# Kernel optimization log

Measured on AMD Instinct MI355X. Metric: run time of the kernel, lower is better.

## Reference

```python
import jax, jax.numpy as jnp
import numpy as np

B, T, I, H, F = 32, 1024, 64, 512, 63
NEG = -1e9


def _init_params(key):
    ks = jax.random.split(key, 16)
    s = 0.02
    p = {}
    # LSTM (pytorch gate order i,f,g,o)
    p['w_ih'] = jax.random.normal(ks[0], (4 * H, I), jnp.float32) * s
    p['w_hh'] = jax.random.normal(ks[1], (4 * H, H), jnp.float32) * s
    p['b_ih'] = jnp.zeros((4 * H,), jnp.float32)
    p['b_hh'] = jnp.zeros((4 * H,), jnp.float32)
    # shared layer
    p['w_sh'] = jax.random.normal(ks[2], (H, H), jnp.float32) * s
    p['b_sh'] = jnp.zeros((H,), jnp.float32)
    # state attention: Linear(H,H) -> tanh -> Linear(H,1)
    p['w_sa'] = jax.random.normal(ks[3], (H, H), jnp.float32) * s
    p['b_sa'] = jnp.zeros((H,), jnp.float32)
    p['v_sa'] = jax.random.normal(ks[4], (1, H), jnp.float32) * s
    p['bv_sa'] = jnp.zeros((1,), jnp.float32)
    # reward attention
    p['w_ra'] = jax.random.normal(ks[5], (H, H), jnp.float32) * s
    p['b_ra'] = jnp.zeros((H,), jnp.float32)
    p['v_ra'] = jax.random.normal(ks[6], (1, H), jnp.float32) * s
    p['bv_ra'] = jnp.zeros((1,), jnp.float32)
    # heads
    p['w_st'] = jax.random.normal(ks[7], (F, H), jnp.float32) * s
    p['b_st'] = jnp.zeros((F,), jnp.float32)
    p['w_rw'] = jax.random.normal(ks[8], (1, H), jnp.float32) * s
    p['b_rw'] = jnp.zeros((1,), jnp.float32)
    return p


def setup_inputs() -> dict:
    key = jax.random.key(0)
    k1, k2, k3, kp = jax.random.split(key, 4)
    inp = {
        'x': jax.random.normal(k1, (B, T, I), jnp.float32),
        'x_lengths': jnp.full((B,), T, dtype=jnp.int64),  # full lengths: pack/pad is identity
        'h0': jax.random.normal(k2, (B, H), jnp.float32),
        'c0': jax.random.normal(k3, (B, H), jnp.float32),
    }
    inp.update(_init_params(kp))
    return inp


def _lstm(x, h0, c0, w_ih, w_hh, b_ih, b_hh):
    # x: [B,T,I] -> outputs [B,T,H], final (h,c)
    def step(carry, xt):
        h, c = carry
        gates = xt @ w_ih.T + h @ w_hh.T + b_ih + b_hh  # [B,4H]
        i, f, g, o = jnp.split(gates, 4, axis=-1)
        c = jax.nn.sigmoid(f) * c + jax.nn.sigmoid(i) * jnp.tanh(g)
        h = jax.nn.sigmoid(o) * jnp.tanh(c)
        return (h, c), h
    (hT, cT), outs = jax.lax.scan(step, (h0, c0), jnp.swapaxes(x, 0, 1))
    return jnp.swapaxes(outs, 0, 1), hT, cT


def _causal_attn(feat, w1, b1, v, bv):
    # additive attention pooling over every causal prefix, vectorized over t.
    e = jnp.tanh(feat @ w1.T + b1) @ v.T + bv        # [B,T,1]
    e = e[..., 0]                                     # [B,T]
    t = feat.shape[1]
    causal = jnp.tril(jnp.ones((t, t), bool))         # [T,T] j<=t
    logits = jnp.where(causal[None], e[:, None, :], NEG)
    w = jax.nn.softmax(logits, axis=-1)               # [B,T,T]
    return jnp.einsum('btj,bjh->bth', w, feat)        # [B,T,H]


def reference(x, x_lengths, h0, c0, w_ih, w_hh, b_ih, b_hh, w_sh, b_sh,
              w_sa, b_sa, v_sa, bv_sa, w_ra, b_ra, v_ra, bv_ra,
              w_st, b_st, w_rw, b_rw):
    r_out, hT, cT = _lstm(x, h0, c0, w_ih, w_hh, b_ih, b_hh)
    shared = r_out @ w_sh.T + b_sh                    # [B,T,H]
    state_ctx = _causal_attn(shared, w_sa, b_sa, v_sa, bv_sa)
    reward_ctx = _causal_attn(shared, w_ra, b_ra, v_ra, bv_ra)
    state_outs = state_ctx @ w_st.T + b_st            # [B,T,F]
    reward_outs = reward_ctx @ w_rw.T + b_rw          # [B,T,1]
    return state_outs, reward_outs, (hT, cT)
```

## Files before the change

### kernel.cpp

```cpp
#include <hip/hip_runtime.h>

#define BB 32
#define TT 1024
#define II 64
#define HH 512
#define FF 63
#define G4H 2048
#define KK 576
#define MM 32768
#define NW 32

#define RW_OFF 2064384
#define HT_OFF 2097152
#define CT_OFF 2113536

#define WS_FLAGS   0
#define WS_FLAG    4096
#define WS_TICK    4224
#define WS_CHOSEN  4288
#define WS_TICK2   4352
#define WS_BIASC   8448
#define WS_BSH     16640
#define WS_BCSA    18688
#define WS_BCRA    20736
#define WS_BCH     22784
#define WS_SCAL    23040
#define WS_VS      23168
#define WS_VR      24192
#define WS_ZB      25216
#define WS_H0      27264
#define WS_CP      60032
#define WS_WHPAD   92800
#define WS_WHC     223872
#define WS_WSHT    354944
#define WS_WSA     879232
#define WS_WRA     1403520
#define WS_WCSA    1927808
#define WS_WCRA    2452096
#define WS_WCAT    2976384
#define WS_XP      5335680
#define WS_ES      9529984
#define WS_ER      9661056
#define WS_PROJ    9792128
#define WS_HX      13986432

typedef __bf16  bf16x8 __attribute__((ext_vector_type(8)));
typedef float   f32x4  __attribute__((ext_vector_type(4)));
typedef uint4 uint4a __attribute__((may_alias));
typedef unsigned int u32;

__device__ __forceinline__ float bf2f(unsigned short u) {
    unsigned int v = ((unsigned int)u) << 16;
    return __builtin_bit_cast(float, v);
}
__device__ __forceinline__ unsigned short f2bf(float f) {
    unsigned int u = __builtin_bit_cast(unsigned int, f);
    u += 0x7fffu + ((u >> 16) & 1u);
    return (unsigned short)(u >> 16);
}
__device__ __forceinline__ bf16x8 ldb8(const unsigned short* p) {
    uint4 v = *(const uint4a*)p;
    return __builtin_bit_cast(bf16x8, v);
}
__device__ __forceinline__ float sigf(float x) { return 1.f / (1.f + __expf(-x)); }
__device__ __forceinline__ float tanhfast(float x) { return 1.f - 2.f / (__expf(2.f * x) + 1.f); }

__device__ __forceinline__ unsigned short loadu(const void* p, int i, int fl) {
    return fl ? f2bf(((const float*)p)[i]) : ((const unsigned short*)p)[i];
}
__device__ __forceinline__ float loadf(const void* p, int i, int fl) {
    return fl ? ((const float*)p)[i] : bf2f(((const unsigned short*)p)[i]);
}

__global__ void sniff_k(const unsigned short* __restrict__ xr, unsigned int* __restrict__ flag) {
    if (threadIdx.x == 0) {
        int cnt = 0;
        for (int i = 0; i < 256; ++i) {
            unsigned short u = xr[i];
            int e = (u >> 7) & 0xFF;
            if (u == 0 || (e >= 100 && e <= 140)) ++cnt;
        }
        *flag = (cnt < 220) ? 1u : 0u;
    }
}

__global__ void prep_all(const void* x, const void* h0, const void* c0,
                         const void* w_sh, const void* w_sa, const void* w_ra,
                         const void* w_st, const void* w_rw,
                         const void* v_sa, const void* v_ra,
                         const void* b_sh, const void* bv_sa, const void* bv_ra,
                         char* ws) {
    const int fl = (int)*(const unsigned int*)(ws + WS_FLAG);
    unsigned short* xp    = (unsigned short*)(ws + WS_XP);
    unsigned short* h0s   = (unsigned short*)(ws + WS_H0);
    unsigned short* cp    = (unsigned short*)(ws + WS_CP);
    unsigned short* wshT  = (unsigned short*)(ws + WS_WSHT);
    unsigned short* wsa   = (unsigned short*)(ws + WS_WSA);
    unsigned short* wra   = (unsigned short*)(ws + WS_WRA);
    unsigned short* whpad = (unsigned short*)(ws + WS_WHPAD);
    unsigned short* vs    = (unsigned short*)(ws + WS_VS);
    unsigned short* vr    = (unsigned short*)(ws + WS_VR);
    float* bsh  = (float*)(ws + WS_BSH);
    float* scal = (float*)(ws + WS_SCAL);
    float* zb   = (float*)(ws + WS_ZB);

    int gt = blockIdx.x * 256 + threadIdx.x;
    int gs = gridDim.x * 256;
    for (int i = gt; i < BB * TT * II; i += gs) xp[i] = loadu(x, i, fl);
    for (int i = gt; i < BB * HH; i += gs) { h0s[i] = loadu(h0, i, fl); cp[i] = loadu(c0, i, fl); }
    for (int i = gt; i < HH * HH; i += gs) {
        int m = i >> 9, k = i & 511;
        wshT[i] = loadu(w_sh, k * HH + m, fl);
        wsa[i] = loadu(w_sa, i, fl);
        wra[i] = loadu(w_ra, i, fl);
    }
    for (int i = gt; i < 128 * HH; i += gs) {
        int f = i >> 9, k = i & 511;
        whpad[i] = (f < FF) ? loadu(w_st, f * HH + k, fl)
                 : (f == FF ? loadu(w_rw, k, fl) : (unsigned short)0);
    }
    for (int i = gt; i < HH; i += gs) {
        vs[i] = loadu(v_sa, i, fl); vr[i] = loadu(v_ra, i, fl);
        bsh[i] = loadf(b_sh, i, fl); zb[i] = 0.f;
    }
    if (gt == 0) { scal[0] = loadf(bv_sa, 0, fl); scal[1] = loadf(bv_ra, 0, fl); }
}

__global__ void prep_w(const void* __restrict__ w_hh, const void* __restrict__ w_ih,
                       const void* __restrict__ b_ih, const void* __restrict__ b_hh,
                       char* ws) {
    const int fl = (int)*(const unsigned int*)(ws + WS_FLAG);
    unsigned short* wcat = (unsigned short*)(ws + WS_WCAT);
    float* biasc = (float*)(ws + WS_BIASC);
    int c = blockIdx.x;
    for (int k = threadIdx.x; k < KK; k += 256)
        wcat[c * KK + k] = (k < HH) ? loadu(w_hh, c * HH + k, fl)
                                    : loadu(w_ih, c * II + (k - HH), fl);
    if (threadIdx.x == 0) biasc[c] = loadf(b_ih, c, fl) + loadf(b_hh, c, fl);
}

__global__ __launch_bounds__(256, 1)
void lstm_k(char* __restrict__ ws, void* __restrict__ dout) {
    __shared__ float gbuf[32][68];
    __shared__ int s_slot;
    __shared__ u32 s_go;
    __shared__ unsigned short As2[128][72];
    __shared__ unsigned short Bs2[64][72];
    __shared__ int s_job;

    u32* tick   = (u32*)(ws + WS_TICK);
    u32* chosen = (u32*)(ws + WS_CHOSEN);

    if (threadIdx.x == 0) {
        u32 xcc;
        asm volatile("s_getreg_b32 %0, hwreg(HW_REG_XCC_ID)" : "=s"(xcc));
        xcc &= 7u;
        int slot = -1;
        u32 tk = __hip_atomic_fetch_add(&tick[xcc], 1u, __ATOMIC_RELAXED,
                                        __HIP_MEMORY_SCOPE_AGENT);
        if (tk < (u32)NW) {
            if (tk == (u32)NW - 1u) {
                u32 expected = 0u;
                __hip_atomic_compare_exchange_strong(chosen, &expected, xcc + 1u,
                    __ATOMIC_RELAXED, __ATOMIC_RELAXED, __HIP_MEMORY_SCOPE_AGENT);
            }
            u32 c = 0u;
            for (int it = 0; it < (1 << 20); ++it) {
                c = __hip_atomic_load(chosen, __ATOMIC_RELAXED, __HIP_MEMORY_SCOPE_AGENT);
                if (c != 0u) break;
                __builtin_amdgcn_s_sleep(8);
            }
            if (c == xcc + 1u) slot = (int)tk;
        }
        s_slot = slot;
        s_go = 0u;
    }
    __syncthreads();
    const int g = s_slot;

    if (g < 0) {
        const int tid = threadIdx.x;
        const int wave = tid >> 6, lane = tid & 63;
        const int quad = lane >> 4, l16 = lane & 15;
        const unsigned short* wshT = (const unsigned short*)(ws + WS_WSHT);
        const float* bsh = (const float*)(ws + WS_BSH);
        for (;;) {
            if (tid == 0)
                s_job = (int)__hip_atomic_fetch_add((u32*)(ws + WS_TICK2), 1u,
                            __ATOMIC_RELAXED, __HIP_MEMORY_SCOPE_AGENT);
            __syncthreads();
            const int job = s_job;
            if (job >= 75) return;
            if (job < 72) {
                const int mb = (job < 64) ? (job >> 3) : 0;
                const int nb = (job < 64) ? (job & 7) : (job - 64);
                const unsigned short* A = (const unsigned short*)
                    (ws + ((job < 64) ? WS_WSA : WS_WHPAD));
                unsigned short* C = (unsigned short*)
                    (ws + ((job < 64) ? WS_WCSA : WS_WHC));
                f32x4 acc[2][4];
#pragma unroll
                for (int tm = 0; tm < 2; ++tm)
#pragma unroll
                    for (int tn = 0; tn < 4; ++tn) acc[tm][tn] = (f32x4){0.f, 0.f, 0.f, 0.f};
                for (int k0 = 0; k0 < 512; k0 += 64) {
#pragma unroll
                    for (int i = 0; i < 4; ++i) {
                        int v = tid + i * 256;
                        int rowa = v >> 3, kc = (v & 7) * 8;
                        *(uint4a*)&As2[rowa][kc] =
                            *(const uint4a*)(A + (mb * 128 + rowa) * 512 + k0 + kc);
                    }
#pragma unroll
                    for (int i = 0; i < 2; ++i) {
                        int v = tid + i * 256;
                        int rowb = v >> 3, kc = (v & 7) * 8;
                        *(uint4a*)&Bs2[rowb][kc] =
                            *(const uint4a*)(wshT + (nb * 64 + rowb) * 512 + k0 + kc);
                    }
                    __syncthreads();
#pragma unroll
                    for (int ks = 0; ks < 2; ++ks) {
                        bf16x8 a0 = ldb8(&As2[wave * 32 + l16][ks * 32 + quad * 8]);
                        bf16x8 a1 = ldb8(&As2[wave * 32 + 16 + l16][ks * 32 + quad * 8]);
#pragma unroll
                        for (int tn = 0; tn < 4; ++tn) {
                            bf16x8 bb = ldb8(&Bs2[tn * 16 + l16][ks * 32 + quad * 8]);
                            acc[0][tn] = __builtin_amdgcn_mfma_f32_16x16x32_bf16(a0, bb, acc[0][tn], 0, 0, 0);
                            acc[1][tn] = __builtin_amdgcn_mfma_f32_16x16x32_bf16(a1, bb, acc[1][tn], 0, 0, 0);
                        }
                    }
                    __syncthreads();
                }
#pragma unroll
                for (int tm = 0; tm < 2; ++tm)
#pragma unroll
                    for (int tn = 0; tn < 4; ++tn)
#pragma unroll
                        for (int r = 0; r < 4; ++r) {
                            int row = mb * 128 + wave * 32 + tm * 16 + quad * 4 + r;
                            int col = nb * 64 + tn * 16 + l16;
                            C[row * 512 + col] = f2bf(acc[tm][tn][r]);
                        }
            } else {
                const int fl = (int)*(const unsigned int*)(ws + WS_FLAG);
                if (job == 72 || job == 73) {
                    const unsigned short* w = (const unsigned short*)
                        (ws + ((job == 72) ? WS_WSA : WS_WRA));
                    const char* b2 = (const char*)0;
                    float* o = (float*)(ws + ((job == 72) ? WS_BCSA : WS_BCRA));
                    (void)b2;
                    for (int j = tid; j < 512; j += 256) {
                        float s = (job == 72) ? ((float*)(ws + WS_SCAL))[0] * 0.f : 0.f;
                        s = 0.f;
                        for (int k = 0; k < HH; ++k) s += bf2f(w[j * HH + k]) * bsh[k];
                        o[j] = s;
                    }
                } else {
                    const unsigned short* w = (const unsigned short*)(ws + WS_WHPAD);
                    float* o = (float*)(ws + WS_BCH);
                    if (tid < 64) {
                        float s = 0.f;
                        for (int k = 0; k < HH; ++k) s += bf2f(w[tid * HH + k]) * bsh[k];
                        o[tid] = s;
                    }
                }
            }
            __syncthreads();
        }
    }

    const unsigned short* xp    = (const unsigned short*)(ws + WS_XP);
    const unsigned short* wcat  = (const unsigned short*)(ws + WS_WCAT);
    const float*          biasc = (const float*)(ws + WS_BIASC);
    const unsigned short* cinit = (const unsigned short*)(ws + WS_CP);
    const unsigned short* h0s   = (const unsigned short*)(ws + WS_H0);
    unsigned short*       hx    = (unsigned short*)(ws + WS_HX);
    u32*                  flags = (u32*)(ws + WS_FLAGS);
    const int fl = (int)*(const unsigned int*)(ws + WS_FLAG);

    const int tid  = threadIdx.x;
    const int wave = tid >> 6, lane = tid & 63;
    const int quad = lane >> 4, l16 = lane & 15;
    const int mh = wave & 1, nh = wave >> 1;
    const int m = mh * 16 + l16;

    bf16x8 bw[2][18];
#pragma unroll
    for (int tn = 0; tn < 2; ++tn) {
        int nl   = nh * 32 + tn * 16 + l16;
        int gcol = (nl >> 4) * HH + g * 16 + (nl & 15);
        const unsigned short* wp = wcat + gcol * KK + quad * 8;
#pragma unroll
        for (int ks = 0; ks < 18; ++ks) bw[tn][ks] = ldb8(wp + ks * 32);
    }

    const int b  = tid >> 3, pr = tid & 7, cc = pr * 2;
    const int n  = g * 16 + cc;
    const float bi0 = biasc[n],          bi1 = biasc[n + 1];
    const float bff0 = biasc[HH + n],    bff1 = biasc[HH + n + 1];
    const float bg0 = biasc[2*HH + n],   bg1 = biasc[2*HH + n + 1];
    const float bo0 = biasc[3*HH + n],   bo1 = biasc[3*HH + n + 1];
    float cst0 = bf2f(cinit[b * HH + n]);
    float cst1 = bf2f(cinit[b * HH + n + 1]);

    const unsigned short* xbase = xp + m * (TT * II) + quad * 8;
    bf16x8 ax0 = ldb8(xbase), ax1 = ldb8(xbase + 32);

    u32* myflag = flags + g * 32;
    u32* pollp  = flags + (lane & 31) * 32;

    for (int t = 0; t < TT; ++t) {
        int tn1 = (t + 1 < TT) ? t + 1 : t;
        bf16x8 axn0 = ldb8(xbase + tn1 * II);
        bf16x8 axn1 = ldb8(xbase + tn1 * II + 32);

        const unsigned short* hrow =
            (t == 0 ? h0s : hx + (t - 1) * (BB * HH)) + m * HH + quad * 8;
        bf16x8 a[16];
#pragma unroll
        for (int i = 0; i < 16; ++i) a[i] = ldb8(hrow + i * 32);

        f32x4 acc0  = {0.f, 0.f, 0.f, 0.f}, acc1  = {0.f, 0.f, 0.f, 0.f};
        f32x4 acc0b = {0.f, 0.f, 0.f, 0.f}, acc1b = {0.f, 0.f, 0.f, 0.f};
        __builtin_amdgcn_s_setprio(1);
        acc0  = __builtin_amdgcn_mfma_f32_16x16x32_bf16(ax0, bw[0][16], acc0,  0, 0, 0);
        acc1  = __builtin_amdgcn_mfma_f32_16x16x32_bf16(ax0, bw[1][16], acc1,  0, 0, 0);
        acc0b = __builtin_amdgcn_mfma_f32_16x16x32_bf16(ax1, bw[0][17], acc0b, 0, 0, 0);
        acc1b = __builtin_amdgcn_mfma_f32_16x16x32_bf16(ax1, bw[1][17], acc1b, 0, 0, 0);
#pragma unroll
        for (int i = 0; i < 8; ++i) {
            acc0  = __builtin_amdgcn_mfma_f32_16x16x32_bf16(a[i],     bw[0][i],     acc0,  0, 0, 0);
            acc1  = __builtin_amdgcn_mfma_f32_16x16x32_bf16(a[i],     bw[1][i],     acc1,  0, 0, 0);
            acc0b = __builtin_amdgcn_mfma_f32_16x16x32_bf16(a[i + 8], bw[0][i + 8], acc0b, 0, 0, 0);
            acc1b = __builtin_amdgcn_mfma_f32_16x16x32_bf16(a[i + 8], bw[1][i + 8], acc1b, 0, 0, 0);
        }
        __builtin_amdgcn_s_setprio(0);
        acc0 = acc0 + acc0b;
        acc1 = acc1 + acc1b;

        {
            int row = mh * 16 + quad * 4;
#pragma unroll
            for (int r = 0; r < 4; ++r) gbuf[row + r][nh * 32 + l16]      = acc0[r];
#pragma unroll
            for (int r = 0; r < 4; ++r) gbuf[row + r][nh * 32 + 16 + l16] = acc1[r];
        }
        __syncthreads();

        {
            float2 giv = *(const float2*)&gbuf[b][cc];
            float2 gfv = *(const float2*)&gbuf[b][16 + cc];
            float2 ggv = *(const float2*)&gbuf[b][32 + cc];
            float2 gov = *(const float2*)&gbuf[b][48 + cc];
            cst0 = sigf(gfv.x + bff0) * cst0 + sigf(giv.x + bi0) * tanhfast(ggv.x + bg0);
            cst1 = sigf(gfv.y + bff1) * cst1 + sigf(giv.y + bi1) * tanhfast(ggv.y + bg1);
            float h0v = sigf(gov.x + bo0) * tanhfast(cst0);
            float h1v = sigf(gov.y + bo1) * tanhfast(cst1);
            u32 hp = (u32)f2bf(h0v) | ((u32)f2bf(h1v) << 16);
            *(u32*)&hx[t * (BB * HH) + b * HH + n] = hp;
            if (t == TT - 1) {
                if (fl) {
                    ((float*)dout)[HT_OFF + b * HH + n]     = h0v;
                    ((float*)dout)[HT_OFF + b * HH + n + 1] = h1v;
                    ((float*)dout)[CT_OFF + b * HH + n]     = cst0;
                    ((float*)dout)[CT_OFF + b * HH + n + 1] = cst1;
                } else {
                    ((u32*)dout)[(HT_OFF + b * HH + n) >> 1] = hp;
                    ((u32*)dout)[(CT_OFF + b * HH + n) >> 1] =
                        (u32)f2bf(cst0) | ((u32)f2bf(cst1) << 16);
                }
            }
        }
        __syncthreads();

        if (tid == 0)
            (void)__hip_atomic_fetch_add(myflag, 1u, __ATOMIC_RELAXED,
                                         __HIP_MEMORY_SCOPE_WORKGROUP);

        u32 die = 0u;
        if (wave == 0) {
            const u32 tgt = (u32)(t + 1);
            int it = 0;
            for (;;) {
                u32 v = (lane < 32)
                    ? __hip_atomic_load(pollp, __ATOMIC_RELAXED, __HIP_MEMORY_SCOPE_AGENT)
                    : tgt;
                if (__all((int)(v >= tgt))) break;
                if (++it > (1 << 17)) { die = 1u; break; }
            }
            if (lane == 0) {
                if (die)
                    __hip_atomic_store(myflag, (u32)(TT + 2), __ATOMIC_RELAXED,
                                       __HIP_MEMORY_SCOPE_AGENT);
                __hip_atomic_store(&s_go, die ? (u32)(TT + 2) : (u32)(t + 1),
                                   __ATOMIC_RELAXED, __HIP_MEMORY_SCOPE_WORKGROUP);
            }
        } else {
            const u32 tgt = (u32)(t + 1);
            int it = 0; u32 v;
            for (;;) {
                v = __hip_atomic_load(&s_go, __ATOMIC_RELAXED,
                                      __HIP_MEMORY_SCOPE_WORKGROUP);
                if (v >= tgt) break;
                if (++it > (1 << 21)) { v = (u32)(TT + 2); break; }
            }
            if (v >= (u32)(TT + 1)) die = 1u;
        }
        if (die) break;
        asm volatile("" ::: "memory");
        ax0 = axn0; ax1 = axn1;
    }
}

__global__ void bias_fix(const void* b_sa, const void* b_ra,
                         const void* b_st, const void* b_rw, char* ws) {
    const int fl = (int)*(const unsigned int*)(ws + WS_FLAG);
    int j = threadIdx.x;
    if (blockIdx.x == 0)      ((float*)(ws + WS_BCSA))[j] += loadf(b_sa, j, fl);
    else if (blockIdx.x == 1) ((float*)(ws + WS_BCRA))[j] += loadf(b_ra, j, fl);
    else if (j < 64)
        ((float*)(ws + WS_BCH))[j] += (j < FF) ? loadf(b_st, j, fl) : loadf(b_rw, 0, fl);
}

__global__ __launch_bounds__(256)
void gemm_tail(const unsigned short* __restrict__ A,
               const unsigned short* __restrict__ Wes,
               const float* __restrict__ bes,
               const unsigned short* __restrict__ vvs,
               float* __restrict__ eout,
               const unsigned short* __restrict__ Wpj,
               const float* __restrict__ bpj,
               unsigned short* __restrict__ proj) {
    __shared__ unsigned short As[128][72];
    __shared__ unsigned short Bs[64][72];
    const int tid = threadIdx.x;
    const int wave = tid >> 6, lane = tid & 63, quad = lane >> 4, l16 = lane & 15;
    const int nb = blockIdx.x, mb = blockIdx.y;
    const bool ispj = (nb == 16);
    const unsigned short* W = ispj ? Wpj : (Wes + nb * 64 * 512);

    f32x4 acc[2][4];
#pragma unroll
    for (int tm = 0; tm < 2; ++tm)
#pragma unroll
        for (int tn = 0; tn < 4; ++tn) acc[tm][tn] = (f32x4){0.f, 0.f, 0.f, 0.f};

    for (int k0 = 0; k0 < 512; k0 += 64) {
#pragma unroll
        for (int i = 0; i < 4; ++i) {
            int v = tid + i * 256;
            int rowa = v >> 3, kc = (v & 7) * 8;
            *(uint4a*)&As[rowa][kc] = *(const uint4a*)(A + (mb * 128 + rowa) * 512 + k0 + kc);
        }
#pragma unroll
        for (int i = 0; i < 2; ++i) {
            int v = tid + i * 256;
            int rowb = v >> 3, kc = (v & 7) * 8;
            *(uint4a*)&Bs[rowb][kc] = *(const uint4a*)(W + rowb * 512 + k0 + kc);
        }
        __syncthreads();
#pragma unroll
        for (int ks = 0; ks < 2; ++ks) {
            bf16x8 a0 = ldb8(&As[wave * 32 + l16][ks * 32 + quad * 8]);
            bf16x8 a1 = ldb8(&As[wave * 32 + 16 + l16][ks * 32 + quad * 8]);
#pragma unroll
            for (int tn = 0; tn < 4; ++tn) {
                bf16x8 bb = ldb8(&Bs[tn * 16 + l16][ks * 32 + quad * 8]);
                acc[0][tn] = __builtin_amdgcn_mfma_f32_16x16x32_bf16(a0, bb, acc[0][tn], 0, 0, 0);
                acc[1][tn] = __builtin_amdgcn_mfma_f32_16x16x32_bf16(a1, bb, acc[1][tn], 0, 0, 0);
            }
        }
        __syncthreads();
    }
    if (ispj) {
#pragma unroll
        for (int tm = 0; tm < 2; ++tm)
#pragma unroll
            for (int tn = 0; tn < 4; ++tn)
#pragma unroll
                for (int r = 0; r < 4; ++r) {
                    int row = mb * 128 + wave * 32 + tm * 16 + quad * 4 + r;
                    int col = tn * 16 + l16;
                    proj[row * 64 + col] = f2bf(acc[tm][tn][r] + bpj[col]);
                }
    } else {
        const int eoff = (nb >= 8) ? MM : 0;
        float vcol[4], bcol[4];
#pragma unroll
        for (int tn = 0; tn < 4; ++tn) {
            int col = nb * 64 + tn * 16 + l16;
            vcol[tn] = bf2f(vvs[col]); bcol[tn] = bes[col];
        }
#pragma unroll
        for (int tm = 0; tm < 2; ++tm)
#pragma unroll
            for (int r = 0; r < 4; ++r) {
                float s = 0.f;
#pragma unroll
                for (int tn = 0; tn < 4; ++tn)
                    s += vcol[tn] * tanhfast(acc[tm][tn][r] + bcol[tn]);
                s += __shfl_xor(s, 1); s += __shfl_xor(s, 2);
                s += __shfl_xor(s, 4); s += __shfl_xor(s, 8);
                if (l16 == 0) {
                    int row = mb * 128 + wave * 32 + tm * 16 + quad * 4 + r;
                    atomicAdd(&eout[eoff + row], s);
                }
            }
    }
}

__global__ __launch_bounds__(64)
void cumsum_k(char* __restrict__ ws, void* __restrict__ dout) {
    const unsigned short* proj = (const unsigned short*)(ws + WS_PROJ);
    const float* es = (const float*)(ws + WS_ES);
    const float* er = (const float*)(ws + WS_ER);
    const float* scal = (const float*)(ws + WS_SCAL);
    const int fl = (int)*(const unsigned int*)(ws + WS_FLAG);
    const int b = blockIdx.x, lane = threadIdx.x;
    const bool isr = (lane == 63);
    const float bv = isr ? scal[1] : scal[0];
    float m_ = -3e38f, d_ = 0.f, n_ = 0.f;
    float pj = bf2f(proj[b * 64 + lane]);
    float e  = (isr ? er[b] : es[b]) + bv;
    for (int t = 0; t < TT; ++t) {
        float pjn = 0.f, en = 0.f;
        if (t + 1 < TT) {
            int rn = (t + 1) * BB + b;
            pjn = bf2f(proj[rn * 64 + lane]);
            en  = (isr ? er[rn] : es[rn]) + bv;
        }
        float mn = fmaxf(m_, e);
        float al = __expf(m_ - mn);
        float p  = __expf(e - mn);
        d_ = d_ * al + p;
        n_ = n_ * al + p * pj;
        m_ = mn;
        float o = n_ / d_;
        int rout = b * TT + t;
        int addr = isr ? (RW_OFF + rout) : (rout * FF + lane);
        if (fl) ((float*)dout)[addr] = o;
        else    ((unsigned short*)dout)[addr] = f2bf(o);
        pj = pjn; e = en;
    }
}

extern "C" void kernel_launch(void* const* d_in, const int* in_sizes, int n_in,
                              void* d_out, int out_size, void* d_ws, size_t ws_size,
                              hipStream_t stream) {
    const void* x    = d_in[0];
    const void* h0   = d_in[2];
    const void* c0   = d_in[3];
    const void* w_ih = d_in[4];
    const void* w_hh = d_in[5];
    const void* b_ih = d_in[6];
    const void* b_hh = d_in[7];
    const void* w_sh = d_in[8];
    const void* b_sh = d_in[9];
    const void* w_sa = d_in[10];
    const void* b_sa = d_in[11];
    const void* v_sa = d_in[12];
    const void* bv_sa= d_in[13];
    const void* w_ra = d_in[14];
    const void* b_ra = d_in[15];
    const void* v_ra = d_in[16];
    const void* bv_ra= d_in[17];
    const void* w_st = d_in[18];
    const void* b_st = d_in[19];
    const void* w_rw = d_in[20];
    const void* b_rw = d_in[21];

    char* ws = (char*)d_ws;
    unsigned short* wcsa  = (unsigned short*)(ws + WS_WCSA);
    unsigned short* whc   = (unsigned short*)(ws + WS_WHC);
    unsigned short* routs = (unsigned short*)(ws + WS_HX);
    unsigned short* proj  = (unsigned short*)(ws + WS_PROJ);
    unsigned short* vs    = (unsigned short*)(ws + WS_VS);
    float* bcsa = (float*)(ws + WS_BCSA);
    float* bch  = (float*)(ws + WS_BCH);
    float* es   = (float*)(ws + WS_ES);

    (void)hipMemsetAsync(d_ws, 0, 8448, stream);
    (void)hipMemsetAsync(ws + WS_ES, 0, 2 * MM * 4, stream);
    sniff_k<<<1, 64, 0, stream>>>((const unsigned short*)x, (unsigned int*)(ws + WS_FLAG));
    prep_all<<<1024, 256, 0, stream>>>(x, h0, c0, w_sh, w_sa, w_ra, w_st, w_rw,
                                       v_sa, v_ra, b_sh, bv_sa, bv_ra, ws);
    prep_w<<<G4H, 256, 0, stream>>>(w_hh, w_ih, b_ih, b_hh, ws);

    lstm_k<<<256, 256, 0, stream>>>(ws, d_out);

    bias_fix<<<3, 512, 0, stream>>>(b_sa, b_ra, b_st, b_rw, ws);

    gemm_tail<<<dim3(17, 256), 256, 0, stream>>>(routs, wcsa, bcsa, vs, es,
                                                 whc, bch, proj);
    cumsum_k<<<BB, 64, 0, stream>>>(ws, d_out);
}
```

Before: 4.024 ms.

## Replace per-step block barrier with per-wave progress flags polled by peers

Each wave now drains its own stores and publishes its step counter to a per-wave flag slot, instead of the whole block hitting __syncthreads and one thread incrementing a shared counter. The poller reads four per-wave flags per peer block with two 64-bit atomic loads and takes the minimum. The goal is to take a block-wide barrier off the serial LSTM recurrence critical path. It depends on the flag layout having four slots per block, which is not visible here and could break initialization or polling if it does not.

```diff
diff --git a/kernel.cpp b/kernel.cpp
--- a/kernel.cpp
+++ b/kernel.cpp
@@ -48,6 +48,7 @@
 typedef float   f32x4  __attribute__((ext_vector_type(4)));
 typedef uint4 uint4a __attribute__((may_alias));
 typedef unsigned int u32;
+typedef unsigned long long u64;
 
 __device__ __forceinline__ float bf2f(unsigned short u) {
     unsigned int v = ((unsigned int)u) << 16;
@@ -243,16 +244,12 @@
                             C[row * 512 + col] = f2bf(acc[tm][tn][r]);
                         }
             } else {
-                const int fl = (int)*(const unsigned int*)(ws + WS_FLAG);
                 if (job == 72 || job == 73) {
                     const unsigned short* w = (const unsigned short*)
                         (ws + ((job == 72) ? WS_WSA : WS_WRA));
-                    const char* b2 = (const char*)0;
                     float* o = (float*)(ws + ((job == 72) ? WS_BCSA : WS_BCRA));
-                    (void)b2;
                     for (int j = tid; j < 512; j += 256) {
-                        float s = (job == 72) ? ((float*)(ws + WS_SCAL))[0] * 0.f : 0.f;
-                        s = 0.f;
+                        float s = 0.f;
                         for (int k = 0; k < HH; ++k) s += bf2f(w[j * HH + k]) * bsh[k];
                         o[j] = s;
                     }
@@ -372,27 +369,38 @@
                 }
             }
         }
-        __syncthreads();
-
-        if (tid == 0)
-            (void)__hip_atomic_fetch_add(myflag, 1u, __ATOMIC_RELAXED,
-                                         __HIP_MEMORY_SCOPE_WORKGROUP);
+
+        asm volatile("s_waitcnt vmcnt(0)" ::: "memory");
+        if (lane == 0)
+            __hip_atomic_store(myflag + wave, (u32)(t + 1), __ATOMIC_RELAXED,
+                               __HIP_MEMORY_SCOPE_AGENT);
 
         u32 die = 0u;
         if (wave == 0) {
             const u32 tgt = (u32)(t + 1);
             int it = 0;
             for (;;) {
-                u32 v = (lane < 32)
-                    ? __hip_atomic_load(pollp, __ATOMIC_RELAXED, __HIP_MEMORY_SCOPE_AGENT)
-                    : tgt;
-                if (__all((int)(v >= tgt))) break;
+                u32 mn = tgt;
+                if (lane < 32) {
+                    const u64* p64 = (const u64*)pollp;
+                    u64 v01 = __hip_atomic_load(p64,     __ATOMIC_RELAXED, __HIP_MEMORY_SCOPE_AGENT);
+                    u64 v23 = __hip_atomic_load(p64 + 1, __ATOMIC_RELAXED, __HIP_MEMORY_SCOPE_AGENT);
+                    u32 a0 = (u32)v01, a1 = (u32)(v01 >> 32);
+                    u32 a2 = (u32)v23, a3 = (u32)(v23 >> 32);
+                    u32 m01 = a0 < a1 ? a0 : a1;
+                    u32 m23 = a2 < a3 ? a2 : a3;
+                    mn = m01 < m23 ? m01 : m23;
+                }
+                if (__all((int)(mn >= tgt))) break;
                 if (++it > (1 << 17)) { die = 1u; break; }
             }
             if (lane == 0) {
-                if (die)
-                    __hip_atomic_store(myflag, (u32)(TT + 2), __ATOMIC_RELAXED,
-                                       __HIP_MEMORY_SCOPE_AGENT);
+                if (die) {
+#pragma unroll
+                    for (int w2 = 0; w2 < 4; ++w2)
+                        __hip_atomic_store(myflag + w2, (u32)(TT + 2),
+                                           __ATOMIC_RELAXED, __HIP_MEMORY_SCOPE_AGENT);
+                }
                 __hip_atomic_store(&s_go, die ? (u32)(TT + 2) : (u32)(t + 1),
                                    __ATOMIC_RELAXED, __HIP_MEMORY_SCOPE_WORKGROUP);
             }
```

Result: slower. 4.464 ms (+10.9%).
